# Kernel tuning notes

Measured on AMD Instinct MI355X. Metric: run time of the kernel, lower is better.

The kernel has to match this reference:

```python
import jax, jax.numpy as jnp
import numpy as np

SIGMA = 32.0
MAGNITUDE = 1.0


def setup_inputs() -> dict:
    key = jax.random.key(0)
    k1, k2, k3 = jax.random.split(key, 3)
    N = 512
    W = 2048
    L = 2048
    init_vectors = jax.random.normal(k1, (2, N), dtype=jnp.float32)
    x_coord = jax.random.randint(k2, (N,), 0, W)
    y_coord = jax.random.randint(k3, (N,), 0, L)
    return {
        "init_vectors": init_vectors,
        "x_coord": x_coord,
        "y_coord": y_coord,
        "width": W,
        "lenth": L,
    }


def reference(init_vectors, x_coord, y_coord, width, lenth):
    # Scale vectors exactly as the torch module: randn / ((lenth+width)/32) * magnitude
    v = init_vectors * (MAGNITUDE / ((lenth + width) / 32.0))  # [2, N]
    inv2s2 = 1.0 / (2.0 * SIGMA * SIGMA)
    xs = jnp.arange(width, dtype=jnp.float32)   # [W]
    ys = jnp.arange(lenth, dtype=jnp.float32)   # [L]
    xc = x_coord.astype(jnp.float32)            # [N]
    yc = y_coord.astype(jnp.float32)            # [N]
    # Gaussian is separable: exp(-(dx^2+dy^2)/2s^2) = exp(-dx^2/2s^2)*exp(-dy^2/2s^2)
    wx = jnp.exp(-((xs[:, None] - xc[None, :]) ** 2) * inv2s2)  # [W, N]
    wy = jnp.exp(-((ys[:, None] - yc[None, :]) ** 2) * inv2s2)  # [L, N]
    # field[c,x,y] = sum_n wx[x,n] * wy[y,n] * v[c,n]
    t = jnp.einsum("xn,cn->cxn", wx, v)          # [2, W, N] (small)
    field = jnp.einsum("cxn,yn->cxy", t, wy)     # [2, W, L]
    return field[None]                            # [1, 2, W, L]
```

## Files before the change

kernel.cpp:

```cpp
#include <hip/hip_runtime.h>
#include <math.h>


#define N_MAX  512
#define TX     32
#define TY     64
#define R_CUT  128.0f
#define BATCH  8

#define EXP2F(x) __builtin_amdgcn_exp2f(x)

__global__ __launch_bounds__(256, 8) void motion_field_kernel(
    const float* __restrict__ init_vectors,
    const int*   __restrict__ x_coord,
    const int*   __restrict__ y_coord,
    const int*   __restrict__ d_width,
    const int*   __restrict__ d_lenth,
    float*       __restrict__ out,
    int N, int W, int L)
{
    __shared__ float s_xc[N_MAX], s_yc[N_MAX], s_v0[N_MAX], s_v1[N_MAX];
    __shared__ short s_list[N_MAX];
    __shared__ int   s_cnt[4];
    __shared__ float s_ex[BATCH][TX], s_ey[BATCH][TY];

    const int tid  = threadIdx.x;
    const int wave = tid >> 6;
    const int lane = tid & 63;

    const float scale = 32.0f / (float)(d_width[0] + d_lenth[0]);

    for (int i = tid; i < N; i += 256) {
        s_xc[i] = (float)x_coord[i];
        s_yc[i] = (float)y_coord[i];
        s_v0[i] = init_vectors[i] * scale;
        s_v1[i] = init_vectors[N + i] * scale;
    }
    __syncthreads();

    const int x0 = blockIdx.x * TX;
    const int y0 = blockIdx.y * TY;
    const float bx_lo = (float)x0 - R_CUT;
    const float bx_hi = (float)(x0 + TX - 1) + R_CUT;
    const float by_lo = (float)y0 - R_CUT;
    const float by_hi = (float)(y0 + TY - 1) + R_CUT;

    int total = 0;
    for (int base_n = 0; base_n < N; base_n += 256) {
        const int n = base_n + tid;
        bool pred = false;
        if (n < N) {
            const float xc = s_xc[n], yc = s_yc[n];
            pred = (xc >= bx_lo) && (xc <= bx_hi) && (yc >= by_lo) && (yc <= by_hi);
        }
        const unsigned long long m = __ballot(pred);
        if (lane == 0) s_cnt[wave] = __popcll(m);
        __syncthreads();
        const int c0 = s_cnt[0], c1 = s_cnt[1], c2 = s_cnt[2], c3 = s_cnt[3];
        int base = total;
        if (wave > 0) base += c0;
        if (wave > 1) base += c1;
        if (wave > 2) base += c2;
        if (pred) {
            const int pos = base + __popcll(m & ((1ULL << lane) - 1ULL));
            s_list[pos] = (short)n;
        }
        total += c0 + c1 + c2 + c3;
        __syncthreads();
    }
    const int M = total;

    const int u = tid >> 4;
    const int v = tid & 15;

    float acc0[2][4], acc1[2][4];
    #pragma unroll
    for (int i = 0; i < 2; ++i)
        #pragma unroll
        for (int j = 0; j < 4; ++j) { acc0[i][j] = 0.f; acc1[i][j] = 0.f; }

    const float C2 = -1.4426950408889634f / 2048.0f;

    for (int m0 = 0; m0 < M; m0 += BATCH) {
        const int B = (M - m0 < BATCH) ? (M - m0) : BATCH;
        for (int s = tid; s < B * TX; s += 256) {
            const int b = s >> 5, r = s & (TX - 1);
            const int n = (int)s_list[m0 + b];
            const float dx = (float)(x0 + r) - s_xc[n];
            s_ex[b][r] = EXP2F(dx * dx * C2);
        }
        for (int s = tid; s < B * TY; s += 256) {
            const int b = s >> 6, r = s & (TY - 1);
            const int n = (int)s_list[m0 + b];
            const float dy = (float)(y0 + r) - s_yc[n];
            s_ey[b][r] = EXP2F(dy * dy * C2);
        }
        __syncthreads();

        for (int b = 0; b < B; ++b) {
            const int n = (int)s_list[m0 + b];
            const float v0 = s_v0[n], v1 = s_v1[n];
            const float2 ex2 = *reinterpret_cast<const float2*>(&s_ex[b][u * 2]);
            const float4 ey4 = *reinterpret_cast<const float4*>(&s_ey[b][v * 4]);
            const float exs[2] = {ex2.x, ex2.y};
            const float eys[4] = {ey4.x, ey4.y, ey4.z, ey4.w};
            #pragma unroll
            for (int i = 0; i < 2; ++i) {
                const float e0 = exs[i] * v0;
                const float e1 = exs[i] * v1;
                #pragma unroll
                for (int j = 0; j < 4; ++j) {
                    acc0[i][j] = fmaf(e0, eys[j], acc0[i][j]);
                    acc1[i][j] = fmaf(e1, eys[j], acc1[i][j]);
                }
            }
        }
        __syncthreads();
    }

    const size_t WL = (size_t)W * (size_t)L;
    const int xb = x0 + u * 2;
    const int yb = y0 + v * 4;
    #pragma unroll
    for (int i = 0; i < 2; ++i) {
        const size_t x = (size_t)(xb + i);
        float4 o0 = make_float4(acc0[i][0], acc0[i][1], acc0[i][2], acc0[i][3]);
        float4 o1 = make_float4(acc1[i][0], acc1[i][1], acc1[i][2], acc1[i][3]);
        *reinterpret_cast<float4*>(&out[x * (size_t)L + (size_t)yb])      = o0;
        *reinterpret_cast<float4*>(&out[WL + x * (size_t)L + (size_t)yb]) = o1;
    }
}

extern "C" void kernel_launch(void* const* d_in, const int* in_sizes, int n_in,
                              void* d_out, int out_size, void* d_ws, size_t ws_size,
                              hipStream_t stream) {
    const float* init_vectors = (const float*)d_in[0];
    const int*   x_coord      = (const int*)d_in[1];
    const int*   y_coord      = (const int*)d_in[2];
    const int*   d_width      = (const int*)d_in[3];
    const int*   d_lenth      = (const int*)d_in[4];
    float*       out          = (float*)d_out;

    const int N = in_sizes[1];
    const int WL = out_size / 2;
    int W = 1;
    while ((long long)W * (long long)W < (long long)WL) W <<= 1;
    const int L = WL / W;

    dim3 grid(W / TX, L / TY);
    dim3 block(256);
    hipLaunchKernelGGL(motion_field_kernel, grid, block, 0, stream,
                       init_vectors, x_coord, y_coord, d_width, d_lenth,
                       out, N, W, L);
}
```

Baseline: 15.49 us.

## Compute Gaussian weights per thread inline instead of staging batches in shared memory

Removes the batched shared-memory staging of x and y Gaussian weights and the two barriers per batch. Each thread now computes its own 2 x-weights and 4 y-weights per point directly. Coordinates are pre-scaled by sqrt(log2(e)/2048) so each exponent needs only a subtract, a square and a native exp2. This trades redundant exp2 work (6 per thread per point instead of shared work) for no synchronisation and no LDS round trips; pre-scaling coordinates adds small rounding differences.

```diff
diff --git a/kernel.cpp b/kernel.cpp
--- a/kernel.cpp
+++ b/kernel.cpp
@@ -6,7 +6,6 @@
 #define TX     32
 #define TY     64
 #define R_CUT  128.0f
-#define BATCH  8
 
 #define EXP2F(x) __builtin_amdgcn_exp2f(x)
 
@@ -22,17 +21,17 @@
     __shared__ float s_xc[N_MAX], s_yc[N_MAX], s_v0[N_MAX], s_v1[N_MAX];
     __shared__ short s_list[N_MAX];
     __shared__ int   s_cnt[4];
-    __shared__ float s_ex[BATCH][TX], s_ey[BATCH][TY];
 
     const int tid  = threadIdx.x;
     const int wave = tid >> 6;
     const int lane = tid & 63;
 
+    const float S = 0.02654008814f;
     const float scale = 32.0f / (float)(d_width[0] + d_lenth[0]);
 
     for (int i = tid; i < N; i += 256) {
-        s_xc[i] = (float)x_coord[i];
-        s_yc[i] = (float)y_coord[i];
+        s_xc[i] = (float)x_coord[i] * S;
+        s_yc[i] = (float)y_coord[i] * S;
         s_v0[i] = init_vectors[i] * scale;
         s_v1[i] = init_vectors[N + i] * scale;
     }
@@ -40,10 +39,10 @@
 
     const int x0 = blockIdx.x * TX;
     const int y0 = blockIdx.y * TY;
-    const float bx_lo = (float)x0 - R_CUT;
-    const float bx_hi = (float)(x0 + TX - 1) + R_CUT;
-    const float by_lo = (float)y0 - R_CUT;
-    const float by_hi = (float)(y0 + TY - 1) + R_CUT;
+    const float bx_lo = ((float)x0 - R_CUT) * S;
+    const float bx_hi = ((float)(x0 + TX - 1) + R_CUT) * S;
+    const float by_lo = ((float)y0 - R_CUT) * S;
+    const float by_hi = ((float)(y0 + TY - 1) + R_CUT) * S;
 
     int total = 0;
     for (int base_n = 0; base_n < N; base_n += 256) {
@@ -72,6 +71,12 @@
 
     const int u = tid >> 4;
     const int v = tid & 15;
+    const float X0 = (float)(x0 + u * 2) * S;
+    const float X1 = X0 + S;
+    const float Y0 = (float)(y0 + v * 4) * S;
+    const float Y1 = Y0 + S;
+    const float Y2 = Y1 + S;
+    const float Y3 = Y2 + S;
 
     float acc0[2][4], acc1[2][4];
     #pragma unroll
@@ -79,43 +84,30 @@
         #pragma unroll
         for (int j = 0; j < 4; ++j) { acc0[i][j] = 0.f; acc1[i][j] = 0.f; }
 
-    const float C2 = -1.4426950408889634f / 2048.0f;
+    #pragma unroll 2
+    for (int m = 0; m < M; ++m) {
+        const int n = (int)s_list[m];
+        const float xc = s_xc[n];
+        const float yc = s_yc[n];
+        const float v0 = s_v0[n];
+        const float v1 = s_v1[n];
 
-    for (int m0 = 0; m0 < M; m0 += BATCH) {
-        const int B = (M - m0 < BATCH) ? (M - m0) : BATCH;
-        for (int s = tid; s < B * TX; s += 256) {
-            const int b = s >> 5, r = s & (TX - 1);
-            const int n = (int)s_list[m0 + b];
-            const float dx = (float)(x0 + r) - s_xc[n];
-            s_ex[b][r] = EXP2F(dx * dx * C2);
+        const float dx0 = X0 - xc, dx1 = X1 - xc;
+        const float ex0 = EXP2F(-(dx0 * dx0));
+        const float ex1 = EXP2F(-(dx1 * dx1));
+        const float dy0 = Y0 - yc, dy1 = Y1 - yc, dy2 = Y2 - yc, dy3 = Y3 - yc;
+        const float ey[4] = { EXP2F(-(dy0 * dy0)), EXP2F(-(dy1 * dy1)),
+                              EXP2F(-(dy2 * dy2)), EXP2F(-(dy3 * dy3)) };
+
+        const float e00 = ex0 * v0, e01 = ex1 * v0;
+        const float e10 = ex0 * v1, e11 = ex1 * v1;
+        #pragma unroll
+        for (int j = 0; j < 4; ++j) {
+            acc0[0][j] = fmaf(e00, ey[j], acc0[0][j]);
+            acc0[1][j] = fmaf(e01, ey[j], acc0[1][j]);
+            acc1[0][j] = fmaf(e10, ey[j], acc1[0][j]);
+            acc1[1][j] = fmaf(e11, ey[j], acc1[1][j]);
         }
-        for (int s = tid; s < B * TY; s += 256) {
-            const int b = s >> 6, r = s & (TY - 1);
-            const int n = (int)s_list[m0 + b];
-            const float dy = (float)(y0 + r) - s_yc[n];
-            s_ey[b][r] = EXP2F(dy * dy * C2);
-        }
-        __syncthreads();
-
-        for (int b = 0; b < B; ++b) {
-            const int n = (int)s_list[m0 + b];
-            const float v0 = s_v0[n], v1 = s_v1[n];
-            const float2 ex2 = *reinterpret_cast<const float2*>(&s_ex[b][u * 2]);
-            const float4 ey4 = *reinterpret_cast<const float4*>(&s_ey[b][v * 4]);
-            const float exs[2] = {ex2.x, ex2.y};
-            const float eys[4] = {ey4.x, ey4.y, ey4.z, ey4.w};
-            #pragma unroll
-            for (int i = 0; i < 2; ++i) {
-                const float e0 = exs[i] * v0;
-                const float e1 = exs[i] * v1;
-                #pragma unroll
-                for (int j = 0; j < 4; ++j) {
-                    acc0[i][j] = fmaf(e0, eys[j], acc0[i][j]);
-                    acc1[i][j] = fmaf(e1, eys[j], acc1[i][j]);
-                }
-            }
-        }
-        __syncthreads();
     }
 
     const size_t WL = (size_t)W * (size_t)L;
```

Result: slower. 18.10 us (+16.9%).

## Reshape tiles to 8x256 and compute y-Gaussians by exponential recurrence

Applied to the files above, without the earlier changes.

Changes the block tile from 32x64 to 8x256, with each thread owning 8 consecutive y outputs in one x row. Coordinates are pre-scaled so the exponent needs no multiply. The y-direction Gaussian weights are generated by a multiplicative recurrence (two exp2 per 8 values instead of eight). Output stores become nontemporal float4 writes. The tall thin tile widens the candidate window along y, so each block may process more sources, and the recurrence adds some floating-point error.

```diff
diff --git a/kernel.cpp b/kernel.cpp
--- a/kernel.cpp
+++ b/kernel.cpp
@@ -3,12 +3,14 @@
 
 
 #define N_MAX  512
-#define TX     32
-#define TY     64
+#define TX     8
+#define TY     256
 #define R_CUT  128.0f
 #define BATCH  8
 
 #define EXP2F(x) __builtin_amdgcn_exp2f(x)
+
+typedef float f4 __attribute__((ext_vector_type(4)));
 
 __global__ __launch_bounds__(256, 8) void motion_field_kernel(
     const float* __restrict__ init_vectors,
@@ -22,17 +24,20 @@
     __shared__ float s_xc[N_MAX], s_yc[N_MAX], s_v0[N_MAX], s_v1[N_MAX];
     __shared__ short s_list[N_MAX];
     __shared__ int   s_cnt[4];
-    __shared__ float s_ex[BATCH][TX], s_ey[BATCH][TY];
+    __shared__ float s_ex[BATCH][TX];
+    __shared__ float s_ey[BATCH][TY];
 
     const int tid  = threadIdx.x;
     const int wave = tid >> 6;
     const int lane = tid & 63;
 
+    const float S = 0.02654008814f;
+    const float RCONST = 0.99902401f;
     const float scale = 32.0f / (float)(d_width[0] + d_lenth[0]);
 
     for (int i = tid; i < N; i += 256) {
-        s_xc[i] = (float)x_coord[i];
-        s_yc[i] = (float)y_coord[i];
+        s_xc[i] = (float)x_coord[i] * S;
+        s_yc[i] = (float)y_coord[i] * S;
         s_v0[i] = init_vectors[i] * scale;
         s_v1[i] = init_vectors[N + i] * scale;
     }
@@ -40,10 +45,10 @@
 
     const int x0 = blockIdx.x * TX;
     const int y0 = blockIdx.y * TY;
-    const float bx_lo = (float)x0 - R_CUT;
-    const float bx_hi = (float)(x0 + TX - 1) + R_CUT;
-    const float by_lo = (float)y0 - R_CUT;
-    const float by_hi = (float)(y0 + TY - 1) + R_CUT;
+    const float bx_lo = ((float)x0 - R_CUT) * S;
+    const float bx_hi = ((float)(x0 + TX - 1) + R_CUT) * S;
+    const float by_lo = ((float)y0 - R_CUT) * S;
+    const float by_hi = ((float)(y0 + TY - 1) + R_CUT) * S;
 
     int total = 0;
     for (int base_n = 0; base_n < N; base_n += 256) {
@@ -70,65 +75,72 @@
     }
     const int M = total;
 
-    const int u = tid >> 4;
-    const int v = tid & 15;
+    const int u  = tid >> 5;
+    const int vv = tid & 31;
+    const float Xu = (float)(x0 + u) * S;
+    const float Yb = (float)(y0 + vv * 8) * S;
 
-    float acc0[2][4], acc1[2][4];
+    float acc0[8], acc1[8];
     #pragma unroll
-    for (int i = 0; i < 2; ++i)
-        #pragma unroll
-        for (int j = 0; j < 4; ++j) { acc0[i][j] = 0.f; acc1[i][j] = 0.f; }
-
-    const float C2 = -1.4426950408889634f / 2048.0f;
+    for (int j = 0; j < 8; ++j) { acc0[j] = 0.f; acc1[j] = 0.f; }
 
     for (int m0 = 0; m0 < M; m0 += BATCH) {
         const int B = (M - m0 < BATCH) ? (M - m0) : BATCH;
-        for (int s = tid; s < B * TX; s += 256) {
-            const int b = s >> 5, r = s & (TX - 1);
+
+        if (tid < B * TX) {
+            const int b = tid >> 3, r = tid & 7;
             const int n = (int)s_list[m0 + b];
-            const float dx = (float)(x0 + r) - s_xc[n];
-            s_ex[b][r] = EXP2F(dx * dx * C2);
+            const float dx = ((float)(x0 + r)) * S - s_xc[n];
+            s_ex[b][r] = EXP2F(-(dx * dx));
         }
-        for (int s = tid; s < B * TY; s += 256) {
-            const int b = s >> 6, r = s & (TY - 1);
-            const int n = (int)s_list[m0 + b];
-            const float dy = (float)(y0 + r) - s_yc[n];
-            s_ey[b][r] = EXP2F(dy * dy * C2);
+        {
+            const int b = tid >> 5;
+            if (b < B) {
+                const int n = (int)s_list[m0 + b];
+                const float yc = s_yc[n];
+                float d0 = Yb - yc;
+                float e  = EXP2F(-(d0 * d0));
+                float g  = EXP2F(-S * (2.0f * d0 + S));
+                float ey[8];
+                #pragma unroll
+                for (int j = 0; j < 8; ++j) {
+                    ey[j] = e;
+                    e *= g;
+                    g *= RCONST;
+                }
+                f4* dst = (f4*)&s_ey[b][vv * 8];
+                dst[0] = (f4){ey[0], ey[1], ey[2], ey[3]};
+                dst[1] = (f4){ey[4], ey[5], ey[6], ey[7]};
+            }
         }
         __syncthreads();
 
         for (int b = 0; b < B; ++b) {
             const int n = (int)s_list[m0 + b];
-            const float v0 = s_v0[n], v1 = s_v1[n];
-            const float2 ex2 = *reinterpret_cast<const float2*>(&s_ex[b][u * 2]);
-            const float4 ey4 = *reinterpret_cast<const float4*>(&s_ey[b][v * 4]);
-            const float exs[2] = {ex2.x, ex2.y};
-            const float eys[4] = {ey4.x, ey4.y, ey4.z, ey4.w};
+            const float exu = s_ex[b][u];
+            const float e0 = exu * s_v0[n];
+            const float e1 = exu * s_v1[n];
+            const f4 eyA = *(const f4*)&s_ey[b][vv * 8];
+            const f4 eyB = *(const f4*)&s_ey[b][vv * 8 + 4];
+            const float eys[8] = {eyA.x, eyA.y, eyA.z, eyA.w,
+                                  eyB.x, eyB.y, eyB.z, eyB.w};
             #pragma unroll
-            for (int i = 0; i < 2; ++i) {
-                const float e0 = exs[i] * v0;
-                const float e1 = exs[i] * v1;
-                #pragma unroll
-                for (int j = 0; j < 4; ++j) {
-                    acc0[i][j] = fmaf(e0, eys[j], acc0[i][j]);
-                    acc1[i][j] = fmaf(e1, eys[j], acc1[i][j]);
-                }
+            for (int j = 0; j < 8; ++j) {
+                acc0[j] = fmaf(e0, eys[j], acc0[j]);
+                acc1[j] = fmaf(e1, eys[j], acc1[j]);
             }
         }
         __syncthreads();
     }
 
     const size_t WL = (size_t)W * (size_t)L;
-    const int xb = x0 + u * 2;
-    const int yb = y0 + v * 4;
-    #pragma unroll
-    for (int i = 0; i < 2; ++i) {
-        const size_t x = (size_t)(xb + i);
-        float4 o0 = make_float4(acc0[i][0], acc0[i][1], acc0[i][2], acc0[i][3]);
-        float4 o1 = make_float4(acc1[i][0], acc1[i][1], acc1[i][2], acc1[i][3]);
-        *reinterpret_cast<float4*>(&out[x * (size_t)L + (size_t)yb])      = o0;
-        *reinterpret_cast<float4*>(&out[WL + x * (size_t)L + (size_t)yb]) = o1;
-    }
+    const size_t base = (size_t)(x0 + u) * (size_t)L + (size_t)(y0 + vv * 8);
+    f4* p00 = (f4*)&out[base];
+    f4* p10 = (f4*)&out[WL + base];
+    __builtin_nontemporal_store((f4){acc0[0], acc0[1], acc0[2], acc0[3]}, p00);
+    __builtin_nontemporal_store((f4){acc0[4], acc0[5], acc0[6], acc0[7]}, p00 + 1);
+    __builtin_nontemporal_store((f4){acc1[0], acc1[1], acc1[2], acc1[3]}, p10);
+    __builtin_nontemporal_store((f4){acc1[4], acc1[5], acc1[6], acc1[7]}, p10 + 1);
 }
 
 extern "C" void kernel_launch(void* const* d_in, const int* in_sizes, int n_in,
```

Result: slower. 18.64 us (+20.4%).
